# Kernel tuning notes

Measured on AMD Instinct MI355X. Metric: run time of the kernel, lower is better.

The kernel has to match this reference:

```python
import jax, jax.numpy as jnp
from jax import lax
import numpy as np

D_MODEL, D_STATE, D_CONV, EXPAND = 256, 16, 4, 2
D_INNER = EXPAND * D_MODEL            # 512
DT_RANK = (D_MODEL + 15) // 16        # 16
B, NVAR, SEG = 4, 32, 96


def _mamba_params(key, scale=0.02):
    ks = jax.random.split(key, 7)
    in_w = jax.random.normal(ks[0], (2 * D_INNER, D_MODEL)) * scale
    conv_w = jax.random.normal(ks[1], (D_INNER, D_CONV)) * scale
    conv_b = jnp.zeros((D_INNER,))
    xproj_w = jax.random.normal(ks[2], (DT_RANK + 2 * D_STATE, D_INNER)) * scale
    dt_w = jax.random.normal(ks[3], (D_INNER, DT_RANK)) * scale
    # bias so softplus(dt_b) ~ dt in [1e-3, 1e-1] (mamba-style init)
    dt = jnp.exp(jax.random.uniform(ks[4], (D_INNER,)) * (np.log(0.1) - np.log(1e-3)) + np.log(1e-3))
    dt_b = dt + jnp.log(-jnp.expm1(-dt))  # inverse softplus
    A_log = jnp.log(jnp.broadcast_to(jnp.arange(1, D_STATE + 1, dtype=jnp.float32), (D_INNER, D_STATE)))
    Dvec = jnp.ones((D_INNER,))
    out_w = jax.random.normal(ks[5], (D_MODEL, D_INNER)) * scale
    return in_w, conv_w, conv_b, xproj_w, dt_w, dt_b, A_log, Dvec, out_w


def setup_inputs() -> dict:
    key = jax.random.key(0)
    kx, kt, kd = jax.random.split(key, 3)
    x = jax.random.normal(kx, (B, NVAR, SEG, D_MODEL), dtype=jnp.float32)
    t = _mamba_params(kt)
    d = _mamba_params(kd)
    names = ["in_w", "conv_w", "conv_b", "xproj_w", "dt_w", "dt_b", "A_log", "D", "out_w"]
    inp = {"x": x}
    inp.update({f"t_{n}": v for n, v in zip(names, t)})
    inp.update({f"d_{n}": v for n, v in zip(names, d)})
    return inp


def _mamba(x, in_w, conv_w, conv_b, xproj_w, dt_w, dt_b, A_log, Dvec, out_w):
    # x: [Bn, L, d_model] -> [Bn, L, d_model]
    Bn, L, _ = x.shape
    xz = jnp.einsum("bld,ed->ble", x, in_w)          # [Bn, L, 2*d_inner]
    xi, z = jnp.split(xz, 2, axis=-1)
    # causal depthwise conv over time
    xi_nc = xi.transpose(0, 2, 1)                     # [Bn, d_inner, L]
    xc = lax.conv_general_dilated(xi_nc, conv_w[:, None, :], (1,),
                                  [(D_CONV - 1, 0)], feature_group_count=D_INNER)
    xc = jax.nn.silu(xc + conv_b[None, :, None]).transpose(0, 2, 1)  # [Bn, L, d_inner]
    dbl = jnp.einsum("ble,fe->blf", xc, xproj_w)      # [Bn, L, dt_rank+2*d_state]
    dt, Bm, Cm = jnp.split(dbl, [DT_RANK, DT_RANK + D_STATE], axis=-1)
    dt = jax.nn.softplus(jnp.einsum("blr,er->ble", dt, dt_w) + dt_b)  # [Bn, L, d_inner]
    A = -jnp.exp(A_log)                               # [d_inner, d_state]

    def step(h, inp):
        dt_t, B_t, C_t, u_t = inp                     # [Bn,dI], [Bn,dS], [Bn,dS], [Bn,dI]
        dA = jnp.exp(dt_t[:, :, None] * A)            # [Bn, d_inner, d_state]
        h = dA * h + dt_t[:, :, None] * B_t[:, None, :] * u_t[:, :, None]
        y = jnp.einsum("bes,bs->be", h, C_t)
        return h, y

    h0 = jnp.zeros((Bn, D_INNER, D_STATE), x.dtype)
    _, ys = lax.scan(step, h0, (dt.transpose(1, 0, 2), Bm.transpose(1, 0, 2),
                                Cm.transpose(1, 0, 2), xc.transpose(1, 0, 2)))
    y = ys.transpose(1, 0, 2) + xc * Dvec             # skip term D*u
    y = y * jax.nn.silu(z)                            # gate
    return jnp.einsum("ble,de->bld", y, out_w)


def reference(x,
              t_in_w, t_conv_w, t_conv_b, t_xproj_w, t_dt_w, t_dt_b, t_A_log, t_D, t_out_w,
              d_in_w, d_conv_w, d_conv_b, d_xproj_w, d_dt_w, d_dt_b, d_A_log, d_D, d_out_w):
    Bb, Dv, S, dm = x.shape
    # stage 1: time-wise scan per variable
    xt = _mamba(x.reshape(Bb * Dv, S, dm),
                t_in_w, t_conv_w, t_conv_b, t_xproj_w, t_dt_w, t_dt_b, t_A_log, t_D, t_out_w)
    xt = xt.reshape(Bb, Dv, S, dm)
    # stage 2: dimension-wise scan per time segment
    xd = _mamba(xt.transpose(0, 2, 1, 3).reshape(Bb * S, Dv, dm),
                d_in_w, d_conv_w, d_conv_b, d_xproj_w, d_dt_w, d_dt_b, d_A_log, d_D, d_out_w)
    return xd.reshape(Bb, S, Dv, dm).transpose(0, 2, 1, 3)
```

## Files before the change

kernel.cpp:

```cpp
#include <hip/hip_runtime.h>
#include <hip/hip_bf16.h>
#include <math.h>

#define D_MODEL 256
#define D_STATE 16
#define D_INNER 512
#define DT_RANK 16
#define NB 4
#define NVAR 32
#define SEG 96
#define TOKENS (NB*NVAR*SEG)

typedef float f4 __attribute__((ext_vector_type(4)));

__device__ __forceinline__ float silu_f(float x) { return x / (1.0f + __expf(-x)); }

__global__ __launch_bounds__(256)
void transpose_w(const float* __restrict__ W, float* __restrict__ WT, int N, int K)
{
    __shared__ float t[32][33];
    const int k0 = blockIdx.x * 32, n0 = blockIdx.y * 32;
    const int tx = threadIdx.x & 31, ty = threadIdx.x >> 5;
#pragma unroll
    for (int i = 0; i < 32; i += 8)
        t[ty + i][tx] = W[(size_t)(n0 + ty + i) * K + k0 + tx];
    __syncthreads();
#pragma unroll
    for (int i = 0; i < 32; i += 8)
        WT[(size_t)(k0 + ty + i) * N + n0 + tx] = t[tx][ty + i];
}

template<int K, int BN, int BK, int MODE>
__global__ __launch_bounds__(256, 4)
void gemm_v6(const float* __restrict__ A, const float* __restrict__ WT,
             float* __restrict__ C, int N)
{
    constexpr int NT  = K / BK;
    constexpr int CPL = BN / 64;
    constexpr int KRD = 1024 / (BN * 4);
    constexpr int J   = BK / (KRD * 4);
    typedef float cvec __attribute__((ext_vector_type(CPL)));
    __shared__ float wlds[2 * BK * BN];

    const int tid  = threadIdx.x;
    const int lane = tid & 63;
    const int wid  = __builtin_amdgcn_readfirstlane(tid >> 6);
    const int m0 = blockIdx.x * 32;
    const int n0 = blockIdx.y * BN;

    const float* Ar[8];
#pragma unroll
    for (int r = 0; r < 8; r++)
        Ar[r] = A + (size_t)(m0 + wid * 8 + r) * K;

    auto stage = [&](int dbuf, int k0) {
#pragma unroll
        for (int j = 0; j < J; j++) {
            int kb   = (wid * J + j) * KRD;
            int krow = kb + ((KRD == 2) ? (lane >> 5) : 0);
            int nofs = ((KRD == 2) ? (lane & 31) : lane) * 4;
            int dstw = __builtin_amdgcn_readfirstlane(dbuf * (BK * BN) + kb * BN);
            __builtin_amdgcn_global_load_lds(
                (const __attribute__((address_space(1))) void*)
                    (WT + (size_t)(k0 + krow) * N + n0 + nofs),
                (__attribute__((address_space(3))) void*)(wlds + dstw), 16, 0, 0);
        }
    };

    float acc[8][CPL];
#pragma unroll
    for (int r = 0; r < 8; r++)
#pragma unroll
        for (int g = 0; g < CPL; g++) acc[r][g] = 0.0f;

    stage(0, 0);
    __syncthreads();

    for (int t = 0; t < NT; t++) {
        const int k0 = t * BK;
        if (t + 1 < NT) stage((t + 1) & 1, k0 + BK);
        const float* Wb = wlds + (t & 1) * (BK * BN);
#pragma unroll
        for (int q = 0; q < BK / 4; q++) {
            f4 a4[8];
#pragma unroll
            for (int r = 0; r < 8; r++)
                a4[r] = *(const f4*)(Ar[r] + k0 + 4 * q);
#pragma unroll
            for (int e = 0; e < 4; e++) {
                cvec wv = *(const cvec*)(Wb + (4 * q + e) * BN + CPL * lane);
#pragma unroll
                for (int r = 0; r < 8; r++)
#pragma unroll
                    for (int g = 0; g < CPL; g++)
                        acc[r][g] = fmaf(a4[r][e], wv[g], acc[r][g]);
            }
        }
        __syncthreads();
    }

#pragma unroll
    for (int r = 0; r < 8; r++) {
        int m = m0 + wid * 8 + r;
        int orow = m;
        if (MODE == 2) {
            int b = m / 3072, rr = m % 3072;
            int v = rr / 96, s = rr % 96;
            orow = (b * 96 + s) * 32 + v;
        } else if (MODE == 3) {
            int b = m / 3072, rr = m % 3072;
            int s = rr / 32, v = rr % 32;
            orow = (b * 32 + v) * 96 + s;
        }
        cvec v;
#pragma unroll
        for (int g = 0; g < CPL; g++) v[g] = acc[r][g];
        *(cvec*)(C + (size_t)orow * N + n0 + CPL * lane) = v;
    }
}

__global__ __launch_bounds__(256)
void xproj_dt(const float* __restrict__ xc,
              const float* __restrict__ xpw,
              const float* __restrict__ dtw,
              const float* __restrict__ dtb,
              float* __restrict__ dbl,
              float* __restrict__ dty,
              int M)
{
    constexpr int BM = 32, BN = 64, BK = 32, TM = 2, TN = 4;
    __shared__ float As[BK][BM + 4];
    __shared__ float Ws[BK][BN + 4];
    __shared__ float dbl_s[BM][52];

    const int tid = threadIdx.x;
    const int tx  = tid % (BN / TN);
    const int ty  = tid / (BN / TN);
    const int m0  = blockIdx.x * BM;

    float acc[TM][TN];
#pragma unroll
    for (int i = 0; i < TM; i++)
#pragma unroll
        for (int j = 0; j < TN; j++) acc[i][j] = 0.0f;

    constexpr int AF4 = (BM * BK) / 1024;
    constexpr int WF4 = (BN * BK) / 1024;
    constexpr int F4R = BK / 4;

    for (int k0 = 0; k0 < 512; k0 += BK) {
#pragma unroll
        for (int c = 0; c < AF4; c++) {
            int idx = tid + c * 256;
            int row = idx / F4R;
            int kc  = (idx % F4R) * 4;
            float4 v = *(const float4*)(xc + (size_t)(m0 + row) * 512 + k0 + kc);
            As[kc + 0][row] = v.x;
            As[kc + 1][row] = v.y;
            As[kc + 2][row] = v.z;
            As[kc + 3][row] = v.w;
        }
#pragma unroll
        for (int c = 0; c < WF4; c++) {
            int idx = tid + c * 256;
            int row = idx / F4R;
            int kc  = (idx % F4R) * 4;
            float4 v;
            if (row < 48) v = *(const float4*)(xpw + (size_t)row * 512 + k0 + kc);
            else          v = make_float4(0.f, 0.f, 0.f, 0.f);
            Ws[kc + 0][row] = v.x;
            Ws[kc + 1][row] = v.y;
            Ws[kc + 2][row] = v.z;
            Ws[kc + 3][row] = v.w;
        }
        __syncthreads();

#pragma unroll
        for (int kk = 0; kk < BK; kk++) {
            float a[TM], w[TN];
#pragma unroll
            for (int i = 0; i < TM; i++) a[i] = As[kk][ty * TM + i];
#pragma unroll
            for (int j = 0; j < TN; j++) w[j] = Ws[kk][tx * TN + j];
#pragma unroll
            for (int i = 0; i < TM; i++)
#pragma unroll
                for (int j = 0; j < TN; j++)
                    acc[i][j] = fmaf(a[i], w[j], acc[i][j]);
        }
        __syncthreads();
    }

#pragma unroll
    for (int i = 0; i < TM; i++) {
        int mr = ty * TM + i;
#pragma unroll
        for (int j = 0; j < TN; j++) {
            int n = tx * TN + j;
            if (n < 48) {
                dbl[(size_t)(m0 + mr) * 48 + n] = acc[i][j];
                dbl_s[mr][n] = acc[i][j];
            }
        }
    }
    __syncthreads();

    f4 wA[4], wB[4];
#pragma unroll
    for (int c = 0; c < 4; c++) {
        wA[c] = *(const f4*)(dtw + (size_t)tid * 16 + 4 * c);
        wB[c] = *(const f4*)(dtw + (size_t)(tid + 256) * 16 + 4 * c);
    }
    const float bA = dtb[tid], bB = dtb[tid + 256];
#pragma unroll 4
    for (int r = 0; r < BM; r++) {
        f4 d[4];
#pragma unroll
        for (int c = 0; c < 4; c++) d[c] = *(const f4*)(&dbl_s[r][4 * c]);
        float vA = bA, vB = bB;
#pragma unroll
        for (int c = 0; c < 4; c++)
#pragma unroll
            for (int e = 0; e < 4; e++) {
                vA = fmaf(d[c][e], wA[c][e], vA);
                vB = fmaf(d[c][e], wB[c][e], vB);
            }
        vA = (vA > 20.0f) ? vA : log1pf(__expf(vA));
        vB = (vB > 20.0f) ? vB : log1pf(__expf(vB));
        dty[(size_t)(m0 + r) * 512 + tid]       = vA;
        dty[(size_t)(m0 + r) * 512 + tid + 256] = vB;
    }
}

__global__ __launch_bounds__(256)
void conv_silu(const float* __restrict__ xz, const float* __restrict__ cw,
               const float* __restrict__ cb, float* __restrict__ xc, int L)
{
    int i  = blockIdx.x * 256 + threadIdx.x;
    int e4 = (i & 127) << 2;
    int t  = i >> 7;
    int l  = t % L;
    const f4 w0 = *(const f4*)(cw + e4 * 4);
    const f4 w1 = *(const f4*)(cw + e4 * 4 + 4);
    const f4 w2 = *(const f4*)(cw + e4 * 4 + 8);
    const f4 w3 = *(const f4*)(cw + e4 * 4 + 12);
    f4 acc = *(const f4*)(cb + e4);
#pragma unroll
    for (int j = 0; j < 4; j++) {
        int li = l - 3 + j;
        if (li >= 0) {
            f4 xv = *(const f4*)(xz + (size_t)(t + li - l) * 1024 + e4);
            acc[0] = fmaf(xv[0], w0[j], acc[0]);
            acc[1] = fmaf(xv[1], w1[j], acc[1]);
            acc[2] = fmaf(xv[2], w2[j], acc[2]);
            acc[3] = fmaf(xv[3], w3[j], acc[3]);
        }
    }
    f4 o;
#pragma unroll
    for (int c = 0; c < 4; c++) o[c] = silu_f(acc[c]);
    *(f4*)(xc + (size_t)t * 512 + e4) = o;
}

__global__ __launch_bounds__(256, 4)
void scan_gate8(float* __restrict__ dty,
                const float* __restrict__ xc,
                const float* __restrict__ xz,
                const float* __restrict__ dbl,
                const float* __restrict__ A_log,
                const float* __restrict__ Dvec,
                int L)
{
    int bn = blockIdx.x >> 2;
    int e  = ((blockIdx.x & 3) << 7) + (threadIdx.x >> 1);
    int sh = (threadIdx.x & 1) << 3;

    float Ae[8], h[8];
#pragma unroll
    for (int s = 0; s < 8; s++) {
        Ae[s] = -__expf(A_log[e * D_STATE + sh + s]);
        h[s]  = 0.0f;
    }
    const float De = Dvec[e];

    const int base = bn * L;
    const int last = base + L - 1;

#define LOADS(tk, dt_, u_, Ba_, Bb_, Ca_, Cb_, z_)                       \
    dt_ = dty[(size_t)(tk) * 512 + e];                                   \
    u_  = xc [(size_t)(tk) * 512 + e];                                   \
    Ba_ = *(const f4*)(dbl + (size_t)(tk) * 48 + 16 + sh);               \
    Bb_ = *(const f4*)(dbl + (size_t)(tk) * 48 + 20 + sh);               \
    Ca_ = *(const f4*)(dbl + (size_t)(tk) * 48 + 32 + sh);               \
    Cb_ = *(const f4*)(dbl + (size_t)(tk) * 48 + 36 + sh);               \
    z_  = xz [(size_t)(tk) * 1024 + 512 + e];

#define COMPUTE(tk, dt_, u_, Ba_, Bb_, Ca_, Cb_, z_)                     \
    {                                                                    \
        float y = 0.0f;                                                  \
        float du = (dt_) * (u_);                                         \
        _Pragma("unroll")                                                \
        for (int s = 0; s < 4; s++) {                                    \
            float dA = __expf((dt_) * Ae[s]);                            \
            h[s] = fmaf(dA, h[s], du * (Ba_)[s]);                        \
            y    = fmaf(h[s], (Ca_)[s], y);                              \
        }                                                                \
        _Pragma("unroll")                                                \
        for (int s = 0; s < 4; s++) {                                    \
            float dA = __expf((dt_) * Ae[4 + s]);                        \
            h[4 + s] = fmaf(dA, h[4 + s], du * (Bb_)[s]);                \
            y        = fmaf(h[4 + s], (Cb_)[s], y);                      \
        }                                                                \
        y += __shfl_xor(y, 1);                                           \
        if (sh == 0)                                                     \
            dty[(size_t)(tk) * 512 + e] = (y + (u_) * De) * silu_f(z_);  \
    }

#define REFILL(slot_tk, dt_, u_, Ba_, Bb_, Ca_, Cb_, z_)                 \
    {                                                                    \
        int tp = (slot_tk) > last ? last : (slot_tk);                    \
        LOADS(tp, dt_, u_, Ba_, Bb_, Ca_, Cb_, z_);                      \
    }

    float dt0, u0, z0, dt1, u1, z1, dt2, u2, z2, dt3, u3, z3;
    f4 Ba0, Bb0, Ca0, Cb0, Ba1, Bb1, Ca1, Cb1;
    f4 Ba2, Bb2, Ca2, Cb2, Ba3, Bb3, Ca3, Cb3;
    LOADS(base,     dt0, u0, Ba0, Bb0, Ca0, Cb0, z0);
    LOADS(base + 1, dt1, u1, Ba1, Bb1, Ca1, Cb1, z1);
    LOADS(base + 2, dt2, u2, Ba2, Bb2, Ca2, Cb2, z2);
    LOADS(base + 3, dt3, u3, Ba3, Bb3, Ca3, Cb3, z3);

    for (int l = 0; l < L; l += 4) {
        int tk = base + l;
        COMPUTE(tk,     dt0, u0, Ba0, Bb0, Ca0, Cb0, z0);
        REFILL(tk + 4,  dt0, u0, Ba0, Bb0, Ca0, Cb0, z0);
        COMPUTE(tk + 1, dt1, u1, Ba1, Bb1, Ca1, Cb1, z1);
        REFILL(tk + 5,  dt1, u1, Ba1, Bb1, Ca1, Cb1, z1);
        COMPUTE(tk + 2, dt2, u2, Ba2, Bb2, Ca2, Cb2, z2);
        REFILL(tk + 6,  dt2, u2, Ba2, Bb2, Ca2, Cb2, z2);
        COMPUTE(tk + 3, dt3, u3, Ba3, Bb3, Ca3, Cb3, z3);
        REFILL(tk + 7,  dt3, u3, Ba3, Bb3, Ca3, Cb3, z3);
    }
#undef LOADS
#undef COMPUTE
#undef REFILL
}

template<int OUTMODE>
static void run_stage(const float* xin,
                      const float* in_wT, const float* conv_w, const float* conv_b,
                      const float* xproj_w, const float* dt_w, const float* dt_b,
                      const float* A_log, const float* Dvec, const float* out_wT,
                      float* xz, float* xc, float* dbl, float* dty, float* outp,
                      int Bn, int L, hipStream_t stream)
{
    const int M = TOKENS;
    gemm_v6<256, 256, 8, 0><<<dim3(M / 32, 1024 / 256), 256, 0, stream>>>(xin, in_wT, xz, 1024);
    conv_silu<<<dim3((M * 128) / 256), 256, 0, stream>>>(xz, conv_w, conv_b, xc, L);
    xproj_dt<<<dim3(M / 32), 256, 0, stream>>>(xc, xproj_w, dt_w, dt_b, dbl, dty, M);
    scan_gate8<<<dim3(Bn * 4), 256, 0, stream>>>(dty, xc, xz, dbl, A_log, Dvec, L);
    gemm_v6<512, 128, 32, OUTMODE><<<dim3(M / 32, 256 / 128), 256, 0, stream>>>(dty, out_wT, outp, 256);
}

extern "C" void kernel_launch(void* const* d_in, const int* in_sizes, int n_in,
                              void* d_out, int out_size, void* d_ws, size_t ws_size,
                              hipStream_t stream)
{
    const float* x = (const float*)d_in[0];
    const float* t_in_w    = (const float*)d_in[1];
    const float* t_conv_w  = (const float*)d_in[2];
    const float* t_conv_b  = (const float*)d_in[3];
    const float* t_xproj_w = (const float*)d_in[4];
    const float* t_dt_w    = (const float*)d_in[5];
    const float* t_dt_b    = (const float*)d_in[6];
    const float* t_A_log   = (const float*)d_in[7];
    const float* t_D       = (const float*)d_in[8];
    const float* t_out_w   = (const float*)d_in[9];
    const float* d_in_w    = (const float*)d_in[10];
    const float* d_conv_w  = (const float*)d_in[11];
    const float* d_conv_b  = (const float*)d_in[12];
    const float* d_xproj_w = (const float*)d_in[13];
    const float* d_dt_w    = (const float*)d_in[14];
    const float* d_dt_b    = (const float*)d_in[15];
    const float* d_A_log   = (const float*)d_in[16];
    const float* d_D       = (const float*)d_in[17];
    const float* d_out_w   = (const float*)d_in[18];

    float* ws  = (float*)d_ws;
    float* xz  = ws;
    float* xc  = xz  + (size_t)TOKENS * 1024;
    float* dbl = xc  + (size_t)TOKENS * 512;
    float* dty = dbl + (size_t)TOKENS * 48;
    float* xt  = dty + (size_t)TOKENS * 512;
    float* t_in_wT  = xt + (size_t)TOKENS * 256;
    float* t_out_wT = t_in_wT  + 262144;
    float* d_in_wT  = t_out_wT + 131072;
    float* d_out_wT = d_in_wT  + 262144;
    const size_t need_bytes =
        ((size_t)TOKENS * (1024 + 512 + 48 + 512 + 256) + 2 * (262144 + 131072)) * 4;
    if (ws_size < need_bytes) return;

    transpose_w<<<dim3(256 / 32, 1024 / 32), 256, 0, stream>>>(t_in_w,  t_in_wT,  1024, 256);
    transpose_w<<<dim3(512 / 32,  256 / 32), 256, 0, stream>>>(t_out_w, t_out_wT,  256, 512);
    transpose_w<<<dim3(256 / 32, 1024 / 32), 256, 0, stream>>>(d_in_w,  d_in_wT,  1024, 256);
    transpose_w<<<dim3(512 / 32,  256 / 32), 256, 0, stream>>>(d_out_w, d_out_wT,  256, 512);

    run_stage<2>(x, t_in_wT, t_conv_w, t_conv_b, t_xproj_w, t_dt_w, t_dt_b,
                 t_A_log, t_D, t_out_wT, xz, xc, dbl, dty, xt,
                 NB * NVAR, SEG, stream);
    run_stage<3>(xt, d_in_wT, d_conv_w, d_conv_b, d_xproj_w, d_dt_w, d_dt_b,
                 d_A_log, d_D, d_out_wT, xz, xc, dbl, dty, (float*)d_out,
                 NB * SEG, NVAR, stream);
}
```

Before: 466.9 us.

## Fuse causal conv+SiLU into xproj and scan kernels, batch weight transposes

Removes the standalone conv_silu kernel and the xc intermediate buffer. The xproj kernel now computes conv+SiLU on the fly from xz while staging its A tile. The scan kernel recomputes the conv from a rolling three-value window kept in registers. The four weight transposes are also merged into two launches using blockIdx.z. This saves a full write and reread of the 512-wide xc tensor and two kernel launches, in exchange for redundant conv arithmetic and four-row xz reads in the xproj tile loads.

```diff
diff --git a/kernel.cpp b/kernel.cpp
--- a/kernel.cpp
+++ b/kernel.cpp
@@ -16,8 +16,12 @@
 __device__ __forceinline__ float silu_f(float x) { return x / (1.0f + __expf(-x)); }
 
 __global__ __launch_bounds__(256)
-void transpose_w(const float* __restrict__ W, float* __restrict__ WT, int N, int K)
-{
+void transpose_w2(const float* __restrict__ W0, float* __restrict__ WT0,
+                  const float* __restrict__ W1, float* __restrict__ WT1,
+                  int N, int K)
+{
+    const float* W  = blockIdx.z ? W1  : W0;
+    float*       WT = blockIdx.z ? WT1 : WT0;
     __shared__ float t[32][33];
     const int k0 = blockIdx.x * 32, n0 = blockIdx.y * 32;
     const int tx = threadIdx.x & 31, ty = threadIdx.x >> 5;
@@ -120,13 +124,15 @@
 }
 
 __global__ __launch_bounds__(256)
-void xproj_dt(const float* __restrict__ xc,
-              const float* __restrict__ xpw,
-              const float* __restrict__ dtw,
-              const float* __restrict__ dtb,
-              float* __restrict__ dbl,
-              float* __restrict__ dty,
-              int M)
+void xproj_dt_conv(const float* __restrict__ xz,
+                   const float* __restrict__ cw,
+                   const float* __restrict__ cb,
+                   const float* __restrict__ xpw,
+                   const float* __restrict__ dtw,
+                   const float* __restrict__ dtb,
+                   float* __restrict__ dbl,
+                   float* __restrict__ dty,
+                   int M, int L)
 {
     constexpr int BM = 32, BN = 64, BK = 32, TM = 2, TN = 4;
     __shared__ float As[BK][BM + 4];
@@ -137,6 +143,12 @@
     const int tx  = tid % (BN / TN);
     const int ty  = tid / (BN / TN);
     const int m0  = blockIdx.x * BM;
+    const int lmb = m0 % L;
+
+    const int s_row = tid >> 3;
+    const int s_kc  = (tid & 7) << 2;
+    const int s_m   = m0 + s_row;
+    const int s_lm  = lmb + s_row;
 
     float acc[TM][TN];
 #pragma unroll
@@ -144,21 +156,30 @@
 #pragma unroll
         for (int j = 0; j < TN; j++) acc[i][j] = 0.0f;
 
-    constexpr int AF4 = (BM * BK) / 1024;
     constexpr int WF4 = (BN * BK) / 1024;
     constexpr int F4R = BK / 4;
 
     for (int k0 = 0; k0 < 512; k0 += BK) {
-#pragma unroll
-        for (int c = 0; c < AF4; c++) {
-            int idx = tid + c * 256;
-            int row = idx / F4R;
-            int kc  = (idx % F4R) * 4;
-            float4 v = *(const float4*)(xc + (size_t)(m0 + row) * 512 + k0 + kc);
-            As[kc + 0][row] = v.x;
-            As[kc + 1][row] = v.y;
-            As[kc + 2][row] = v.z;
-            As[kc + 3][row] = v.w;
+        {
+            const int col0 = k0 + s_kc;
+            f4 xv[4];
+#pragma unroll
+            for (int j = 0; j < 4; j++) {
+                if (s_lm - 3 + j >= 0)
+                    xv[j] = *(const f4*)(xz + (size_t)(s_m - 3 + j) * 1024 + col0);
+                else
+                    xv[j] = (f4)0.0f;
+            }
+            f4 bv = *(const f4*)(cb + col0);
+#pragma unroll
+            for (int c = 0; c < 4; c++) {
+                f4 w = *(const f4*)(cw + (size_t)(col0 + c) * 4);
+                float v = bv[c];
+#pragma unroll
+                for (int j = 0; j < 4; j++)
+                    v = fmaf(xv[j][c], w[j], v);
+                As[s_kc + c][s_row] = silu_f(v);
+            }
         }
 #pragma unroll
         for (int c = 0; c < WF4; c++) {
@@ -232,44 +253,15 @@
     }
 }
 
-__global__ __launch_bounds__(256)
-void conv_silu(const float* __restrict__ xz, const float* __restrict__ cw,
-               const float* __restrict__ cb, float* __restrict__ xc, int L)
-{
-    int i  = blockIdx.x * 256 + threadIdx.x;
-    int e4 = (i & 127) << 2;
-    int t  = i >> 7;
-    int l  = t % L;
-    const f4 w0 = *(const f4*)(cw + e4 * 4);
-    const f4 w1 = *(const f4*)(cw + e4 * 4 + 4);
-    const f4 w2 = *(const f4*)(cw + e4 * 4 + 8);
-    const f4 w3 = *(const f4*)(cw + e4 * 4 + 12);
-    f4 acc = *(const f4*)(cb + e4);
-#pragma unroll
-    for (int j = 0; j < 4; j++) {
-        int li = l - 3 + j;
-        if (li >= 0) {
-            f4 xv = *(const f4*)(xz + (size_t)(t + li - l) * 1024 + e4);
-            acc[0] = fmaf(xv[0], w0[j], acc[0]);
-            acc[1] = fmaf(xv[1], w1[j], acc[1]);
-            acc[2] = fmaf(xv[2], w2[j], acc[2]);
-            acc[3] = fmaf(xv[3], w3[j], acc[3]);
-        }
-    }
-    f4 o;
-#pragma unroll
-    for (int c = 0; c < 4; c++) o[c] = silu_f(acc[c]);
-    *(f4*)(xc + (size_t)t * 512 + e4) = o;
-}
-
 __global__ __launch_bounds__(256, 4)
-void scan_gate8(float* __restrict__ dty,
-                const float* __restrict__ xc,
-                const float* __restrict__ xz,
-                const float* __restrict__ dbl,
-                const float* __restrict__ A_log,
-                const float* __restrict__ Dvec,
-                int L)
+void scan_gate8c(float* __restrict__ dty,
+                 const float* __restrict__ xz,
+                 const float* __restrict__ dbl,
+                 const float* __restrict__ cw,
+                 const float* __restrict__ cb,
+                 const float* __restrict__ A_log,
+                 const float* __restrict__ Dvec,
+                 int L)
 {
     int bn = blockIdx.x >> 2;
     int e  = ((blockIdx.x & 3) << 7) + (threadIdx.x >> 1);
@@ -281,24 +273,34 @@
         Ae[s] = -__expf(A_log[e * D_STATE + sh + s]);
         h[s]  = 0.0f;
     }
-    const float De = Dvec[e];
+    const float De  = Dvec[e];
+    const f4 cwe    = *(const f4*)(cw + (size_t)e * 4);
+    const float cbe = cb[e];
+    float w0 = 0.f, w1 = 0.f, w2 = 0.f;
 
     const int base = bn * L;
     const int last = base + L - 1;
 
-#define LOADS(tk, dt_, u_, Ba_, Bb_, Ca_, Cb_, z_)                       \
+#define LOADS(tk, dt_, xi_, Ba_, Bb_, Ca_, Cb_, z_)                      \
     dt_ = dty[(size_t)(tk) * 512 + e];                                   \
-    u_  = xc [(size_t)(tk) * 512 + e];                                   \
+    xi_ = xz [(size_t)(tk) * 1024 + e];                                  \
     Ba_ = *(const f4*)(dbl + (size_t)(tk) * 48 + 16 + sh);               \
     Bb_ = *(const f4*)(dbl + (size_t)(tk) * 48 + 20 + sh);               \
     Ca_ = *(const f4*)(dbl + (size_t)(tk) * 48 + 32 + sh);               \
     Cb_ = *(const f4*)(dbl + (size_t)(tk) * 48 + 36 + sh);               \
     z_  = xz [(size_t)(tk) * 1024 + 512 + e];
 
-#define COMPUTE(tk, dt_, u_, Ba_, Bb_, Ca_, Cb_, z_)                     \
+#define COMPUTE(tk, dt_, xi_, Ba_, Bb_, Ca_, Cb_, z_)                    \
     {                                                                    \
+        float u = cbe;                                                   \
+        u = fmaf(w0, cwe[0], u);                                         \
+        u = fmaf(w1, cwe[1], u);                                         \
+        u = fmaf(w2, cwe[2], u);                                         \
+        u = fmaf(xi_, cwe[3], u);                                        \
+        u = silu_f(u);                                                   \
+        w0 = w1; w1 = w2; w2 = xi_;                                      \
         float y = 0.0f;                                                  \
-        float du = (dt_) * (u_);                                         \
+        float du = (dt_) * u;                                            \
         _Pragma("unroll")                                                \
         for (int s = 0; s < 4; s++) {                                    \
             float dA = __expf((dt_) * Ae[s]);                            \
@@ -313,33 +315,33 @@
         }                                                                \
         y += __shfl_xor(y, 1);                                           \
         if (sh == 0)                                                     \
-            dty[(size_t)(tk) * 512 + e] = (y + (u_) * De) * silu_f(z_);  \
-    }
-
-#define REFILL(slot_tk, dt_, u_, Ba_, Bb_, Ca_, Cb_, z_)                 \
+            dty[(size_t)(tk) * 512 + e] = (y + u * De) * silu_f(z_);     \
+    }
+
+#define REFILL(slot_tk, dt_, xi_, Ba_, Bb_, Ca_, Cb_, z_)                \
     {                                                                    \
         int tp = (slot_tk) > last ? last : (slot_tk);                    \
-        LOADS(tp, dt_, u_, Ba_, Bb_, Ca_, Cb_, z_);                      \
-    }
-
-    float dt0, u0, z0, dt1, u1, z1, dt2, u2, z2, dt3, u3, z3;
+        LOADS(tp, dt_, xi_, Ba_, Bb_, Ca_, Cb_, z_);                     \
+    }
+
+    float dt0, x0, z0, dt1, x1, z1, dt2, x2, z2, dt3, x3, z3;
     f4 Ba0, Bb0, Ca0, Cb0, Ba1, Bb1, Ca1, Cb1;
     f4 Ba2, Bb2, Ca2, Cb2, Ba3, Bb3, Ca3, Cb3;
-    LOADS(base,     dt0, u0, Ba0, Bb0, Ca0, Cb0, z0);
-    LOADS(base + 1, dt1, u1, Ba1, Bb1, Ca1, Cb1, z1);
-    LOADS(base + 2, dt2, u2, Ba2, Bb2, Ca2, Cb2, z2);
-    LOADS(base + 3, dt3, u3, Ba3, Bb3, Ca3, Cb3, z3);
+    LOADS(base,     dt0, x0, Ba0, Bb0, Ca0, Cb0, z0);
+    LOADS(base + 1, dt1, x1, Ba1, Bb1, Ca1, Cb1, z1);
+    LOADS(base + 2, dt2, x2, Ba2, Bb2, Ca2, Cb2, z2);
+    LOADS(base + 3, dt3, x3, Ba3, Bb3, Ca3, Cb3, z3);
 
     for (int l = 0; l < L; l += 4) {
         int tk = base + l;
-        COMPUTE(tk,     dt0, u0, Ba0, Bb0, Ca0, Cb0, z0);
-        REFILL(tk + 4,  dt0, u0, Ba0, Bb0, Ca0, Cb0, z0);
-        COMPUTE(tk + 1, dt1, u1, Ba1, Bb1, Ca1, Cb1, z1);
-        REFILL(tk + 5,  dt1, u1, Ba1, Bb1, Ca1, Cb1, z1);
-        COMPUTE(tk + 2, dt2, u2, Ba2, Bb2, Ca2, Cb2, z2);
-        REFILL(tk + 6,  dt2, u2, Ba2, Bb2, Ca2, Cb2, z2);
-        COMPUTE(tk + 3, dt3, u3, Ba3, Bb3, Ca3, Cb3, z3);
-        REFILL(tk + 7,  dt3, u3, Ba3, Bb3, Ca3, Cb3, z3);
+        COMPUTE(tk,     dt0, x0, Ba0, Bb0, Ca0, Cb0, z0);
+        REFILL(tk + 4,  dt0, x0, Ba0, Bb0, Ca0, Cb0, z0);
+        COMPUTE(tk + 1, dt1, x1, Ba1, Bb1, Ca1, Cb1, z1);
+        REFILL(tk + 5,  dt1, x1, Ba1, Bb1, Ca1, Cb1, z1);
+        COMPUTE(tk + 2, dt2, x2, Ba2, Bb2, Ca2, Cb2, z2);
+        REFILL(tk + 6,  dt2, x2, Ba2, Bb2, Ca2, Cb2, z2);
+        COMPUTE(tk + 3, dt3, x3, Ba3, Bb3, Ca3, Cb3, z3);
+        REFILL(tk + 7,  dt3, x3, Ba3, Bb3, Ca3, Cb3, z3);
     }
 #undef LOADS
 #undef COMPUTE
@@ -351,14 +353,15 @@
                       const float* in_wT, const float* conv_w, const float* conv_b,
                       const float* xproj_w, const float* dt_w, const float* dt_b,
                       const float* A_log, const float* Dvec, const float* out_wT,
-                      float* xz, float* xc, float* dbl, float* dty, float* outp,
+                      float* xz, float* dbl, float* dty, float* outp,
                       int Bn, int L, hipStream_t stream)
 {
     const int M = TOKENS;
     gemm_v6<256, 256, 8, 0><<<dim3(M / 32, 1024 / 256), 256, 0, stream>>>(xin, in_wT, xz, 1024);
-    conv_silu<<<dim3((M * 128) / 256), 256, 0, stream>>>(xz, conv_w, conv_b, xc, L);
-    xproj_dt<<<dim3(M / 32), 256, 0, stream>>>(xc, xproj_w, dt_w, dt_b, dbl, dty, M);
-    scan_gate8<<<dim3(Bn * 4), 256, 0, stream>>>(dty, xc, xz, dbl, A_log, Dvec, L);
+    xproj_dt_conv<<<dim3(M / 32), 256, 0, stream>>>(
+        xz, conv_w, conv_b, xproj_w, dt_w, dt_b, dbl, dty, M, L);
+    scan_gate8c<<<dim3(Bn * 4), 256, 0, stream>>>(dty, xz, dbl, conv_w, conv_b,
+                                                  A_log, Dvec, L);
     gemm_v6<512, 128, 32, OUTMODE><<<dim3(M / 32, 256 / 128), 256, 0, stream>>>(dty, out_wT, outp, 256);
 }
 
@@ -388,8 +391,7 @@
 
     float* ws  = (float*)d_ws;
     float* xz  = ws;
-    float* xc  = xz  + (size_t)TOKENS * 1024;
-    float* dbl = xc  + (size_t)TOKENS * 512;
+    float* dbl = xz  + (size_t)TOKENS * 1024;
     float* dty = dbl + (size_t)TOKENS * 48;
     float* xt  = dty + (size_t)TOKENS * 512;
     float* t_in_wT  = xt + (size_t)TOKENS * 256;
@@ -397,18 +399,18 @@
     float* d_in_wT  = t_out_wT + 131072;
     float* d_out_wT = d_in_wT  + 262144;
     const size_t need_bytes =
-        ((size_t)TOKENS * (1024 + 512 + 48 + 512 + 256) + 2 * (262144 + 131072)) * 4;
+        ((size_t)TOKENS * (1024 + 48 + 512 + 256) + 2 * (262144 + 131072)) * 4;
     if (ws_size < need_bytes) return;
 
-    transpose_w<<<dim3(256 / 32, 1024 / 32), 256, 0, stream>>>(t_in_w,  t_in_wT,  1024, 256);
-    transpose_w<<<dim3(512 / 32,  256 / 32), 256, 0, stream>>>(t_out_w, t_out_wT,  256, 512);
-    transpose_w<<<dim3(256 / 32, 1024 / 32), 256, 0, stream>>>(d_in_w,  d_in_wT,  1024, 256);
-    transpose_w<<<dim3(512 / 32,  256 / 32), 256, 0, stream>>>(d_out_w, d_out_wT,  256, 512);
+    transpose_w2<<<dim3(256 / 32, 1024 / 32, 2), 256, 0, stream>>>(
+        t_in_w, t_in_wT, d_in_w, d_in_wT, 1024, 256);
+    transpose_w2<<<dim3(512 / 32, 256 / 32, 2), 256, 0, stream>>>(
+        t_out_w, t_out_wT, d_out_w, d_out_wT, 256, 512);
 
     run_stage<2>(x, t_in_wT, t_conv_w, t_conv_b, t_xproj_w, t_dt_w, t_dt_b,
-                 t_A_log, t_D, t_out_wT, xz, xc, dbl, dty, xt,
+                 t_A_log, t_D, t_out_wT, xz, dbl, dty, xt,
                  NB * NVAR, SEG, stream);
     run_stage<3>(xt, d_in_wT, d_conv_w, d_conv_b, d_xproj_w, d_dt_w, d_dt_b,
-                 d_A_log, d_D, d_out_wT, xz, xc, dbl, dty, (float*)d_out,
+                 d_A_log, d_D, d_out_wT, xz, dbl, dty, (float*)d_out,
                  NB * SEG, NVAR, stream);
 }
```

New measurement: 456.4 us. 2.2% less time.
